# Kernel optimization log

Hardware: AMD Instinct MI355X
Metric: run time of the kernel (lower is better)

Reference implementation:

```python
import jax, jax.numpy as jnp
import numpy as np

B, N = 32, 1024


def _pose(points, rot, trans):
    # points: [B,N,3], rot: [B,3,3], trans: [B,3]
    # torch.bmm(points, rot.transpose(1,2)) + trans.unsqueeze(1)
    return jnp.einsum('bni,bji->bnj', points, rot) + trans[:, None, :]


def _l2_dis(pred, target):
    # [B,N] pointwise L2 distance
    return jnp.linalg.norm(pred - target, axis=2)


def _cd_dis(pred, target):
    # symmetric Chamfer-style distance, [B,N]
    p2 = jnp.sum(pred * pred, axis=2)          # [B,N]
    t2 = jnp.sum(target * target, axis=2)      # [B,N]
    cross = jnp.einsum('bnd,bmd->bnm', pred, target)  # [B,N,N]
    d2 = jnp.maximum(p2[:, :, None] + t2[:, None, :] - 2.0 * cross, 0.0)
    dis = jnp.sqrt(d2)                          # [B,N,N]
    dis1 = jnp.min(dis, axis=2)                 # min over target -> [B,N]
    dis2 = jnp.min(dis, axis=1)                 # min over pred   -> [B,N]
    return 0.5 * (dis1 + dis2)


def setup_inputs() -> dict:
    key = jax.random.key(0)
    ks = jax.random.split(key, 8)
    return {
        'delta_rot_pred': jax.random.normal(ks[0], (B, 3, 3), jnp.float32),
        'delta_trans_pred': jax.random.normal(ks[1], (B, 3), jnp.float32),
        'trans_cur': jax.random.normal(ks[2], (B, 3), jnp.float32),
        'rot_cur': jax.random.normal(ks[3], (B, 3, 3), jnp.float32),
        'rot_gt': jax.random.normal(ks[4], (B, 3, 3), jnp.float32),
        'trans_gt': jax.random.normal(ks[5], (B, 3), jnp.float32),
        'points_tmp': jax.random.normal(ks[6], (B, N, 3), jnp.float32),
        'sym_flag': jax.random.uniform(ks[7], (B,), jnp.float32),
    }


def reference(delta_rot_pred, delta_trans_pred, trans_cur, rot_cur, rot_gt, trans_gt, points_tmp, sym_flag):
    posed_pred = _pose(points_tmp, delta_rot_pred, delta_trans_pred)   # [B,N,3]
    posed_gt = _pose(points_tmp, rot_gt, trans_gt)                     # [B,N,3]
    posed_refined = _pose(posed_pred, rot_cur, trans_cur)              # [B,N,3]
    l2 = _l2_dis(posed_refined, posed_gt)                              # [B,N]
    cd = _cd_dis(posed_refined, posed_gt)                              # [B,N]
    per_point = (1.0 - sym_flag)[:, None] * l2 + sym_flag[:, None] * cd
    loss_pose = per_point.mean(axis=1).mean()
    return loss_pose
```

## Files before the change

### kernel.cpp

```cpp
#include <hip/hip_runtime.h>
#include <math.h>

constexpr int B = 32;
constexpr int N = 1024;
constexpr int S = 32;
constexpr int R = N / S;
constexpr int NBLK = B * S;
constexpr int NTHR = 256;
constexpr int RPT = 8;
constexpr int CHUNKS = 32;
constexpr int CPC = N / CHUNKS;

__global__ __launch_bounds__(NTHR, 4) void chamfer_main(
    const float* __restrict__ dR,
    const float* __restrict__ dt,
    const float* __restrict__ tc,
    const float* __restrict__ Rc,
    const float* __restrict__ G,
    const float* __restrict__ g,
    const float* __restrict__ pts,
    const float* __restrict__ sym,
    float* __restrict__ partial)
{
    __shared__ float4 sp[N];
    __shared__ float4 sg[N];
    __shared__ float wsum[NTHR / 64];

    const int blk   = blockIdx.x;
    const int b     = blk / S;
    const int slice = blk % S;
    const int t     = threadIdx.x;

    const float* dRb = dR + b * 9;
    const float* Rcb = Rc + b * 9;
    const float* Gb  = G  + b * 9;
    const float* dtb = dt + b * 3;
    const float* tcb = tc + b * 3;
    const float* gb  = g  + b * 3;
    const float symb = sym[b];

    float M[9], v[3];
    #pragma unroll
    for (int j = 0; j < 3; ++j) {
        #pragma unroll
        for (int i = 0; i < 3; ++i) {
            M[j*3+i] = Rcb[j*3+0] * dRb[0*3+i]
                     + Rcb[j*3+1] * dRb[1*3+i]
                     + Rcb[j*3+2] * dRb[2*3+i];
        }
        v[j] = Rcb[j*3+0] * dtb[0] + Rcb[j*3+1] * dtb[1] + Rcb[j*3+2] * dtb[2] + tcb[j];
    }

    float acc = 0.f;

    #pragma unroll
    for (int i = t; i < N; i += NTHR) {
        const float* p = pts + ((size_t)b * N + i) * 3;
        const float px = p[0], py = p[1], pz = p[2];
        const float ax = M[0]*px + M[1]*py + M[2]*pz + v[0];
        const float ay = M[3]*px + M[4]*py + M[5]*pz + v[1];
        const float az = M[6]*px + M[7]*py + M[8]*pz + v[2];
        const float cx = Gb[0]*px + Gb[1]*py + Gb[2]*pz + gb[0];
        const float cy = Gb[3]*px + Gb[4]*py + Gb[5]*pz + gb[1];
        const float cz = Gb[6]*px + Gb[7]*py + Gb[8]*pz + gb[2];
        sp[i] = make_float4(ax, ay, az, ax*ax + ay*ay + az*az);
        sg[i] = make_float4(cx, cy, cz, cx*cx + cy*cy + cz*cz);
        if (slice == 0) {
            const float dx = ax - cx, dy = ay - cy, dz = az - cz;
            acc += (1.f - symb) * sqrtf(dx*dx + dy*dy + dz*dz);
        }
    }
    __syncthreads();

    const int side  = t >> 7;
    const int ti    = t & 127;
    const int chunk = ti & (CHUNKS - 1);
    const int group = ti >> 5;
    const int r0    = slice * R + group * RPT;

    const float4* own = side ? sg : sp;
    const float4* opp = side ? sp : sg;

    float nx[RPT], ny[RPT], nz[RPT], p2[RPT];
    #pragma unroll
    for (int r = 0; r < RPT; ++r) {
        const float4 o = own[r0 + r];
        nx[r] = -2.f * o.x;
        ny[r] = -2.f * o.y;
        nz[r] = -2.f * o.z;
        p2[r] = o.w;
    }

    const float4* qp = opp + chunk * CPC;
    float mins[RPT];
    #pragma unroll
    for (int r = 0; r < RPT; ++r) mins[r] = 3.4e38f;

    #pragma unroll 8
    for (int k = 0; k < CPC; ++k) {
        const int kk = (k + chunk) & (CPC - 1);
        const float4 q = qp[kk];
        #pragma unroll
        for (int r = 0; r < RPT; ++r) {
            const float f = fmaf(nx[r], q.x, fmaf(ny[r], q.y, fmaf(nz[r], q.z, q.w)));
            mins[r] = fminf(mins[r], f);
        }
    }

    #pragma unroll
    for (int r = 0; r < RPT; ++r) {
        #pragma unroll
        for (int m = 1; m <= 16; m <<= 1)
            mins[r] = fminf(mins[r], __shfl_xor(mins[r], m));
    }
    if ((ti & 31) == 0) {
        #pragma unroll
        for (int r = 0; r < RPT; ++r) {
            const float d2 = fmaxf(mins[r] + p2[r], 0.f);
            acc += 0.5f * symb * sqrtf(d2);
        }
    }

    #pragma unroll
    for (int m = 1; m <= 32; m <<= 1) acc += __shfl_xor(acc, m);
    if ((t & 63) == 0) wsum[t >> 6] = acc;
    __syncthreads();
    if (t == 0) partial[blk] = (wsum[0] + wsum[1]) + (wsum[2] + wsum[3]);
}

__global__ __launch_bounds__(256) void chamfer_final(
    const float* __restrict__ partial, float* __restrict__ out)
{
    __shared__ float wsum[4];
    const int t = threadIdx.x;
    const float4 v = ((const float4*)partial)[t];
    float a = (v.x + v.y) + (v.z + v.w);
    #pragma unroll
    for (int m = 1; m <= 32; m <<= 1) a += __shfl_xor(a, m);
    if ((t & 63) == 0) wsum[t >> 6] = a;
    __syncthreads();
    if (t == 0) out[0] = ((wsum[0] + wsum[1]) + (wsum[2] + wsum[3])) * (1.0f / (float)(B * N));
}

extern "C" void kernel_launch(void* const* d_in, const int* in_sizes, int n_in,
                              void* d_out, int out_size, void* d_ws, size_t ws_size,
                              hipStream_t stream) {
    const float* dR  = (const float*)d_in[0];
    const float* dt  = (const float*)d_in[1];
    const float* tc  = (const float*)d_in[2];
    const float* Rc  = (const float*)d_in[3];
    const float* G   = (const float*)d_in[4];
    const float* g   = (const float*)d_in[5];
    const float* pts = (const float*)d_in[6];
    const float* sym = (const float*)d_in[7];

    float* partial = (float*)d_ws;
    float* out     = (float*)d_out;

    chamfer_main<<<NBLK, NTHR, 0, stream>>>(dR, dt, tc, Rc, G, g, pts, sym, partial);
    chamfer_final<<<1, 256, 0, stream>>>(partial, out);
}
```

Baseline: 17.49 us.

## Fuse final reduction via atomic counter, pack FMAs, vectorize point loads

Merges the second reduction kernel into the main kernel: each block publishes its partial sum, and the last block to arrive, detected through an atomic counter, does the final sum. The counter is zeroed with a memset before launch. The inner chamfer loop now evaluates two rows per instruction with packed v_pk_fma_f32 inline assembly, and the target index changes from a rotated chunk to a strided layout. Points are loaded as three float4 per thread instead of scalar loads. This removes a kernel launch and cuts VALU instruction count, at the cost of a memset launch, atomic traffic and hand-written assembly operand selects.

Result: slower. 44.40 us (+153.8%).

```diff
diff --git a/kernel.cpp b/kernel.cpp
--- a/kernel.cpp
+++ b/kernel.cpp
@@ -11,7 +11,7 @@
 constexpr int CHUNKS = 32;
 constexpr int CPC = N / CHUNKS;
 
-__global__ __launch_bounds__(NTHR, 4) void chamfer_main(
+__global__ __launch_bounds__(NTHR, 4) void chamfer_fused(
     const float* __restrict__ dR,
     const float* __restrict__ dt,
     const float* __restrict__ tc,
@@ -20,11 +20,14 @@
     const float* __restrict__ g,
     const float* __restrict__ pts,
     const float* __restrict__ sym,
-    float* __restrict__ partial)
+    float* __restrict__ partial,
+    unsigned int* __restrict__ counter,
+    float* __restrict__ out)
 {
     __shared__ float4 sp[N];
     __shared__ float4 sg[N];
-    __shared__ float wsum[NTHR / 64];
+    __shared__ float wsum[4];
+    __shared__ int lastflag;
 
     const int blk   = blockIdx.x;
     const int b     = blk / S;
@@ -53,21 +56,29 @@
 
     float acc = 0.f;
 
-    #pragma unroll
-    for (int i = t; i < N; i += NTHR) {
-        const float* p = pts + ((size_t)b * N + i) * 3;
-        const float px = p[0], py = p[1], pz = p[2];
-        const float ax = M[0]*px + M[1]*py + M[2]*pz + v[0];
-        const float ay = M[3]*px + M[4]*py + M[5]*pz + v[1];
-        const float az = M[6]*px + M[7]*py + M[8]*pz + v[2];
-        const float cx = Gb[0]*px + Gb[1]*py + Gb[2]*pz + gb[0];
-        const float cy = Gb[3]*px + Gb[4]*py + Gb[5]*pz + gb[1];
-        const float cz = Gb[6]*px + Gb[7]*py + Gb[8]*pz + gb[2];
-        sp[i] = make_float4(ax, ay, az, ax*ax + ay*ay + az*az);
-        sg[i] = make_float4(cx, cy, cz, cx*cx + cy*cy + cz*cz);
-        if (slice == 0) {
-            const float dx = ax - cx, dy = ay - cy, dz = az - cz;
-            acc += (1.f - symb) * sqrtf(dx*dx + dy*dy + dz*dz);
+    {
+        const float4* P4 = (const float4*)(pts + (size_t)b * N * 3);
+        const float4 A  = P4[3*t + 0];
+        const float4 Bv = P4[3*t + 1];
+        const float4 C  = P4[3*t + 2];
+        const float px[4] = {A.x, A.w, Bv.z, C.y};
+        const float py[4] = {A.y, Bv.x, Bv.w, C.z};
+        const float pz[4] = {A.z, Bv.y, C.x, C.w};
+        #pragma unroll
+        for (int u = 0; u < 4; ++u) {
+            const int i = 4*t + u;
+            const float ax = M[0]*px[u] + M[1]*py[u] + M[2]*pz[u] + v[0];
+            const float ay = M[3]*px[u] + M[4]*py[u] + M[5]*pz[u] + v[1];
+            const float az = M[6]*px[u] + M[7]*py[u] + M[8]*pz[u] + v[2];
+            const float cx = Gb[0]*px[u] + Gb[1]*py[u] + Gb[2]*pz[u] + gb[0];
+            const float cy = Gb[3]*px[u] + Gb[4]*py[u] + Gb[5]*pz[u] + gb[1];
+            const float cz = Gb[6]*px[u] + Gb[7]*py[u] + Gb[8]*pz[u] + gb[2];
+            sp[i] = make_float4(ax, ay, az, ax*ax + ay*ay + az*az);
+            sg[i] = make_float4(cx, cy, cz, cx*cx + cy*cy + cz*cz);
+            if (slice == 0) {
+                const float dx = ax - cx, dy = ay - cy, dz = az - cz;
+                acc += (1.f - symb) * sqrtf(dx*dx + dy*dy + dz*dz);
+            }
         }
     }
     __syncthreads();
@@ -80,33 +91,44 @@
 
     const float4* own = side ? sg : sp;
     const float4* opp = side ? sp : sg;
+    const float4* qp  = opp + chunk;
 
-    float nx[RPT], ny[RPT], nz[RPT], p2[RPT];
+    float2 nx2[RPT/2], ny2[RPT/2], nz2[RPT/2], mins2[RPT/2];
+    float p2[RPT];
     #pragma unroll
-    for (int r = 0; r < RPT; ++r) {
-        const float4 o = own[r0 + r];
-        nx[r] = -2.f * o.x;
-        ny[r] = -2.f * o.y;
-        nz[r] = -2.f * o.z;
-        p2[r] = o.w;
+    for (int i = 0; i < RPT/2; ++i) {
+        const float4 o0 = own[r0 + 2*i];
+        const float4 o1 = own[r0 + 2*i + 1];
+        nx2[i] = make_float2(-2.f * o0.x, -2.f * o1.x);
+        ny2[i] = make_float2(-2.f * o0.y, -2.f * o1.y);
+        nz2[i] = make_float2(-2.f * o0.z, -2.f * o1.z);
+        p2[2*i]   = o0.w;
+        p2[2*i+1] = o1.w;
+        mins2[i] = make_float2(3.4e38f, 3.4e38f);
     }
-
-    const float4* qp = opp + chunk * CPC;
-    float mins[RPT];
-    #pragma unroll
-    for (int r = 0; r < RPT; ++r) mins[r] = 3.4e38f;
 
     #pragma unroll 8
     for (int k = 0; k < CPC; ++k) {
-        const int kk = (k + chunk) & (CPC - 1);
-        const float4 q = qp[kk];
+        const float4 q = qp[k * CHUNKS];
+        const float2 qxy = make_float2(q.x, q.y);
+        const float2 qzw = make_float2(q.z, q.w);
         #pragma unroll
-        for (int r = 0; r < RPT; ++r) {
-            const float f = fmaf(nx[r], q.x, fmaf(ny[r], q.y, fmaf(nz[r], q.z, q.w)));
-            mins[r] = fminf(mins[r], f);
+        for (int i = 0; i < RPT/2; ++i) {
+            float2 f2;
+            asm("v_pk_fma_f32 %0, %1, %2, %3 op_sel:[0,0,1] op_sel_hi:[1,0,1]"
+                : "=v"(f2) : "v"(nz2[i]), "v"(qzw), "v"(qzw));
+            asm("v_pk_fma_f32 %0, %1, %2, %0 op_sel:[0,1,0] op_sel_hi:[1,1,1]"
+                : "+v"(f2) : "v"(ny2[i]), "v"(qxy));
+            asm("v_pk_fma_f32 %0, %1, %2, %0 op_sel:[0,0,0] op_sel_hi:[1,0,1]"
+                : "+v"(f2) : "v"(nx2[i]), "v"(qxy));
+            mins2[i].x = fminf(mins2[i].x, f2.x);
+            mins2[i].y = fminf(mins2[i].y, f2.y);
         }
     }
 
+    float mins[RPT];
+    #pragma unroll
+    for (int i = 0; i < RPT/2; ++i) { mins[2*i] = mins2[i].x; mins[2*i+1] = mins2[i].y; }
     #pragma unroll
     for (int r = 0; r < RPT; ++r) {
         #pragma unroll
@@ -125,21 +147,28 @@
     for (int m = 1; m <= 32; m <<= 1) acc += __shfl_xor(acc, m);
     if ((t & 63) == 0) wsum[t >> 6] = acc;
     __syncthreads();
-    if (t == 0) partial[blk] = (wsum[0] + wsum[1]) + (wsum[2] + wsum[3]);
-}
+    if (t == 0) {
+        const float bsum = (wsum[0] + wsum[1]) + (wsum[2] + wsum[3]);
+        __hip_atomic_store(&partial[blk], bsum, __ATOMIC_RELEASE, __HIP_MEMORY_SCOPE_AGENT);
+        const unsigned old = __hip_atomic_fetch_add(counter, 1u, __ATOMIC_ACQ_REL,
+                                                    __HIP_MEMORY_SCOPE_AGENT);
+        lastflag = (old == (unsigned)(NBLK - 1));
+    }
+    __syncthreads();
 
-__global__ __launch_bounds__(256) void chamfer_final(
-    const float* __restrict__ partial, float* __restrict__ out)
-{
-    __shared__ float wsum[4];
-    const int t = threadIdx.x;
-    const float4 v = ((const float4*)partial)[t];
-    float a = (v.x + v.y) + (v.z + v.w);
-    #pragma unroll
-    for (int m = 1; m <= 32; m <<= 1) a += __shfl_xor(a, m);
-    if ((t & 63) == 0) wsum[t >> 6] = a;
-    __syncthreads();
-    if (t == 0) out[0] = ((wsum[0] + wsum[1]) + (wsum[2] + wsum[3])) * (1.0f / (float)(B * N));
+    if (lastflag) {
+        float a = 0.f;
+        #pragma unroll
+        for (int j = 0; j < NBLK / NTHR; ++j)
+            a += __hip_atomic_load(&partial[t + j * NTHR], __ATOMIC_ACQUIRE,
+                                   __HIP_MEMORY_SCOPE_AGENT);
+        #pragma unroll
+        for (int m = 1; m <= 32; m <<= 1) a += __shfl_xor(a, m);
+        if ((t & 63) == 0) wsum[t >> 6] = a;
+        __syncthreads();
+        if (t == 0)
+            out[0] = ((wsum[0] + wsum[1]) + (wsum[2] + wsum[3])) * (1.0f / (float)(B * N));
+    }
 }
 
 extern "C" void kernel_launch(void* const* d_in, const int* in_sizes, int n_in,
@@ -154,9 +183,11 @@
     const float* pts = (const float*)d_in[6];
     const float* sym = (const float*)d_in[7];
 
-    float* partial = (float*)d_ws;
-    float* out     = (float*)d_out;
+    float* partial       = (float*)d_ws;
+    unsigned int* counter = (unsigned int*)((char*)d_ws + 4096);
+    float* out           = (float*)d_out;
 
-    chamfer_main<<<NBLK, NTHR, 0, stream>>>(dR, dt, tc, Rc, G, g, pts, sym, partial);
-    chamfer_final<<<1, 256, 0, stream>>>(partial, out);
+    hipMemsetAsync(counter, 0, sizeof(unsigned int), stream);
+    chamfer_fused<<<NBLK, NTHR, 0, stream>>>(dR, dt, tc, Rc, G, g, pts, sym,
+                                             partial, counter, out);
 }
```
